# Kernel optimization log

Hardware: AMD Instinct MI355X
Metric: run time of the kernel (lower is better)

## Reference

```python
import jax, jax.numpy as jnp
import numpy as np

B, N, DIM, H, DH = 4, 2048, 768, 12, 64

def layer_norm_no_affine(x, eps=1e-5):
    mu = jnp.mean(x, axis=-1, keepdims=True)
    var = jnp.var(x, axis=-1, keepdims=True)
    return (x - mu) / jnp.sqrt(var + eps)

def setup_inputs() -> dict:
    key = jax.random.key(0)
    ks = jax.random.split(key, 6)
    s = 1.0 / np.sqrt(DIM)
    return {
        "x": jax.random.normal(ks[0], (B, N, DIM), dtype=jnp.float32),
        "gamma": jnp.zeros((DIM,), dtype=jnp.float32),
        "Wq": jax.random.normal(ks[1], (DIM, DIM), dtype=jnp.float32) * s,
        "Wk": jax.random.normal(ks[2], (DIM, DIM), dtype=jnp.float32) * s,
        "Wv": jax.random.normal(ks[3], (DIM, DIM), dtype=jnp.float32) * s,
        "Wo": jax.random.normal(ks[4], (DIM, DIM), dtype=jnp.float32) * s,
    }

def reference(x, gamma, Wq, Wk, Wv, Wo):
    scale = DH ** -0.5
    xn = layer_norm_no_affine(x) * (gamma + 1.0)  # [b,n,dim]
    # projections (torch Linear: y = x @ W.T), split heads b n (h d) -> b h n d
    def proj(t, W):
        return (t @ W.T).reshape(B, N, H, DH).transpose(0, 2, 1, 3)
    q = proj(xn, Wq) * scale
    k = proj(xn, Wk)
    v = proj(xn, Wv)
    qk_sim = jnp.einsum('bhid,bhjd->bhij', q, k)  # full N x N scores (unfused)
    attn = jax.nn.softmax(qk_sim, axis=-1)
    out = jnp.einsum('bhij,bhjd->bhid', attn, v)
    out = out.transpose(0, 2, 1, 3).reshape(B, N, H * DH)
    return out @ Wo.T
```

## Files before the change

kernel.cpp:

```cpp
#include <hip/hip_runtime.h>
#include <stdint.h>

#define NSEQ 2048
#define NB 4
#define NH 12
#define MTOT 8192
#define DMODEL 768

typedef __attribute__((ext_vector_type(8))) short bfx8;
typedef __attribute__((ext_vector_type(4))) float fx4;
typedef __attribute__((ext_vector_type(16))) float fx16;

static __device__ __forceinline__ unsigned short f2bf(float f) {
  union { float f; unsigned u; } v; v.f = f;
  unsigned r = v.u + 0x7FFFu + ((v.u >> 16) & 1u);
  return (unsigned short)(r >> 16);
}

static __device__ __forceinline__ unsigned cvt_pk_bf16(float lo, float hi) {
  unsigned r;
  asm("v_cvt_pk_bf16_f32 %0, %1, %2" : "=v"(r) : "v"(lo), "v"(hi));
  return r;
}

static __device__ __forceinline__ void gload_lds16(const void* g, void* l) {
  __builtin_amdgcn_global_load_lds(
      (const __attribute__((address_space(1))) unsigned int*)g,
      (__attribute__((address_space(3))) unsigned int*)l, 16, 0, 0);
}

__global__ __launch_bounds__(256) void k_ln(const float* __restrict__ x,
                                            const float* __restrict__ gamma,
                                            unsigned short* __restrict__ xn) {
  int row = blockIdx.x * 4 + (threadIdx.x >> 6);
  int lane = threadIdx.x & 63;
  const float* xr = x + (size_t)row * DMODEL;
  float4 a = *(const float4*)(xr + lane * 4);
  float4 b = *(const float4*)(xr + 256 + lane * 4);
  float4 c = *(const float4*)(xr + 512 + lane * 4);
  float s  = a.x + a.y + a.z + a.w + b.x + b.y + b.z + b.w + c.x + c.y + c.z + c.w;
  float ss = a.x*a.x + a.y*a.y + a.z*a.z + a.w*a.w
           + b.x*b.x + b.y*b.y + b.z*b.z + b.w*b.w
           + c.x*c.x + c.y*c.y + c.z*c.z + c.w*c.w;
  #pragma unroll
  for (int off = 1; off < 64; off <<= 1) {
    s  += __shfl_xor(s, off);
    ss += __shfl_xor(ss, off);
  }
  float mu = s * (1.0f / 768.0f);
  float var = ss * (1.0f / 768.0f) - mu * mu;
  float rs = rsqrtf(var + 1e-5f);
  float4 ga = *(const float4*)(gamma + lane * 4);
  float4 gb = *(const float4*)(gamma + 256 + lane * 4);
  float4 gc = *(const float4*)(gamma + 512 + lane * 4);
  unsigned short* orow = xn + (size_t)row * DMODEL;
  ushort4 o;
  o.x = f2bf((a.x - mu) * rs * (ga.x + 1.0f));
  o.y = f2bf((a.y - mu) * rs * (ga.y + 1.0f));
  o.z = f2bf((a.z - mu) * rs * (ga.z + 1.0f));
  o.w = f2bf((a.w - mu) * rs * (ga.w + 1.0f));
  *(ushort4*)(orow + lane * 4) = o;
  o.x = f2bf((b.x - mu) * rs * (gb.x + 1.0f));
  o.y = f2bf((b.y - mu) * rs * (gb.y + 1.0f));
  o.z = f2bf((b.z - mu) * rs * (gb.z + 1.0f));
  o.w = f2bf((b.w - mu) * rs * (gb.w + 1.0f));
  *(ushort4*)(orow + 256 + lane * 4) = o;
  o.x = f2bf((c.x - mu) * rs * (gc.x + 1.0f));
  o.y = f2bf((c.y - mu) * rs * (gc.y + 1.0f));
  o.z = f2bf((c.z - mu) * rs * (gc.z + 1.0f));
  o.w = f2bf((c.w - mu) * rs * (gc.w + 1.0f));
  *(ushort4*)(orow + 512 + lane * 4) = o;
}

__global__ __launch_bounds__(256) void k_wconv(const float* __restrict__ w0,
                                               const float* __restrict__ w1,
                                               const float* __restrict__ w2,
                                               const float* __restrict__ w3,
                                               unsigned short* __restrict__ dst) {
  int which = blockIdx.y;
  const float* src = (which == 0) ? w0 : (which == 1) ? w1 : (which == 2) ? w2 : w3;
  size_t idx = ((size_t)blockIdx.x * 256 + threadIdx.x) * 4;
  float4 v = *(const float4*)(src + idx);
  ushort4 o;
  o.x = f2bf(v.x); o.y = f2bf(v.y); o.z = f2bf(v.z); o.w = f2bf(v.w);
  *(ushort4*)(dst + (size_t)which * (DMODEL * DMODEL) + idx) = o;
}

template<int MODE>
__global__ __launch_bounds__(256) void k_gemm(const unsigned short* __restrict__ A,
                                              const unsigned short* __restrict__ Bbase,
                                              unsigned short* __restrict__ q_o,
                                              unsigned short* __restrict__ k_o,
                                              unsigned short* __restrict__ v_o,
                                              float* __restrict__ f_o) {
  __shared__ unsigned short At[128 * 32];
  __shared__ unsigned short Bt[128 * 32];
  int t = threadIdx.x;
  int w = t >> 6, lane = t & 63;
  int wr = w >> 1, wc = w & 1;
  int g = lane >> 4, cc = lane & 15;
  int mbase = blockIdx.x * 128;
  int by = blockIdx.y;
  const unsigned short* Bp;
  int ncolbase;
  if (MODE == 0) {
    int which = by / 6;
    Bp = Bbase + (size_t)which * (DMODEL * DMODEL);
    ncolbase = (by % 6) * 128;
  } else {
    Bp = Bbase;
    ncolbase = by * 128;
  }
  int srow = lane >> 2;
  int schunk = (lane & 3) * 8;
  const unsigned short* Asrc = A  + (size_t)(mbase   + w * 32 + srow) * DMODEL + schunk;
  const unsigned short* Bsrc = Bp + (size_t)(ncolbase + w * 32 + srow) * DMODEL + schunk;
  unsigned short* Adst0 = At + (w * 32) * 32;
  unsigned short* Bdst0 = Bt + (w * 32) * 32;

  fx4 acc[4][4];
  #pragma unroll
  for (int i = 0; i < 4; ++i)
    #pragma unroll
    for (int j = 0; j < 4; ++j)
      acc[i][j] = (fx4){0.f, 0.f, 0.f, 0.f};

  for (int ks = 0; ks < DMODEL; ks += 32) {
    __syncthreads();
    gload_lds16(Asrc + ks,                    Adst0);
    gload_lds16(Asrc + ks + 16 * DMODEL,      Adst0 + 16 * 32);
    gload_lds16(Bsrc + ks,                    Bdst0);
    gload_lds16(Bsrc + ks + 16 * DMODEL,      Bdst0 + 16 * 32);
    __syncthreads();
    bfx8 af[4], bfr[4];
    #pragma unroll
    for (int mi = 0; mi < 4; ++mi)
      af[mi] = *(const bfx8*)(At + (wr * 64 + mi * 16 + cc) * 32 + g * 8);
    #pragma unroll
    for (int ni = 0; ni < 4; ++ni)
      bfr[ni] = *(const bfx8*)(Bt + (wc * 64 + ni * 16 + cc) * 32 + g * 8);
    #pragma unroll
    for (int mi = 0; mi < 4; ++mi)
      #pragma unroll
      for (int ni = 0; ni < 4; ++ni)
        acc[mi][ni] = __builtin_amdgcn_mfma_f32_16x16x32_bf16(af[mi], bfr[ni], acc[mi][ni], 0, 0, 0);
  }

  if (MODE == 0) {
    int which = by / 6;
    if (which < 2) {
      unsigned short* dst = (which == 0) ? q_o : k_o;
      float fs = (which == 0) ? 0.18033688f : 1.0f;
      #pragma unroll
      for (int mi = 0; mi < 4; ++mi) {
        #pragma unroll
        for (int ni = 0; ni < 4; ++ni) {
          int n = (by % 6) * 128 + wc * 64 + ni * 16 + cc;
          int h = n >> 6, dd = n & 63;
          #pragma unroll
          for (int r = 0; r < 4; ++r) {
            int m = mbase + wr * 64 + mi * 16 + g * 4 + r;
            int bb = m >> 11, nq = m & 2047;
            dst[((size_t)(bb * NH + h) * NSEQ + nq) * 64 + dd] = f2bf(acc[mi][ni][r] * fs);
          }
        }
      }
    } else {
      #pragma unroll
      for (int mi = 0; mi < 4; ++mi) {
        #pragma unroll
        for (int ni = 0; ni < 4; ++ni) {
          int n = (by % 6) * 128 + wc * 64 + ni * 16 + cc;
          int h = n >> 6, dd = n & 63;
          int m0 = mbase + wr * 64 + mi * 16 + g * 4;
          int bb = m0 >> 11, nq = m0 & 2047;
          ushort4 pk;
          pk.x = f2bf(acc[mi][ni][0]);
          pk.y = f2bf(acc[mi][ni][1]);
          pk.z = f2bf(acc[mi][ni][2]);
          pk.w = f2bf(acc[mi][ni][3]);
          *(ushort4*)(v_o + ((size_t)(bb * NH + h) * 64 + dd) * NSEQ + nq) = pk;
        }
      }
    }
  } else {
    #pragma unroll
    for (int mi = 0; mi < 4; ++mi)
      #pragma unroll
      for (int ni = 0; ni < 4; ++ni) {
        int n = by * 128 + wc * 64 + ni * 16 + cc;
        #pragma unroll
        for (int r = 0; r < 4; ++r) {
          int m = mbase + wr * 64 + mi * 16 + g * 4 + r;
          f_o[(size_t)m * DMODEL + n] = acc[mi][ni][r];
        }
      }
  }
}

__global__ __launch_bounds__(256, 3) void k_attn(const unsigned short* __restrict__ qw,
                                                 const unsigned short* __restrict__ kw,
                                                 const unsigned short* __restrict__ vtw,
                                                 unsigned short* __restrict__ ao) {
  __shared__ unsigned short Kb[2][64 * 64];
  __shared__ unsigned short Vb[2][64 * 64];
  int bid = blockIdx.x;
  int xcd = bid & 7, jj = bid >> 3;
  int bh = xcd * 6 + (jj >> 4);
  int qt = jj & 15;
  int t = threadIdx.x;
  int w = t >> 6, lane = t & 63;
  int c = lane & 31, b5 = lane >> 5;
  int q0 = qt * 128 + w * 32;
  const unsigned short* qp = qw + (size_t)bh * NSEQ * 64;
  const unsigned char* kby = (const unsigned char*)(kw  + (size_t)bh * NSEQ * 64);
  const unsigned char* vby = (const unsigned char*)(vtw + (size_t)bh * 64 * NSEQ);

  int srow = lane >> 3;
  int scol = (((lane & 7) ^ srow) << 4);
  int ch0 = 2 * w, ch1 = 2 * w + 1;

  auto stage = [&](int tt, int buf) {
    gload_lds16(kby + (size_t)(tt * 64 + ch0 * 8 + srow) * 128 + scol, &Kb[buf][ch0 * 512]);
    gload_lds16(kby + (size_t)(tt * 64 + ch1 * 8 + srow) * 128 + scol, &Kb[buf][ch1 * 512]);
    gload_lds16(vby + (size_t)(ch0 * 8 + srow) * 4096 + tt * 128 + scol, &Vb[buf][ch0 * 512]);
    gload_lds16(vby + (size_t)(ch1 * 8 + srow) * 4096 + tt * 128 + scol, &Vb[buf][ch1 * 512]);
  };

  bfx8 qf[4];
  #pragma unroll
  for (int dc = 0; dc < 4; ++dc)
    qf[dc] = *(const bfx8*)(qp + (size_t)(q0 + c) * 64 + dc * 16 + b5 * 8);

  fx16 o0, o1;
  #pragma unroll
  for (int i = 0; i < 16; ++i) { o0[i] = 0.f; o1[i] = 0.f; }
  float l_run = 0.f;

  int rsw = (c & 7) << 4;

  stage(0, 0);

  for (int tt = 0; tt < 32; ++tt) {
    int buf = tt & 1;
    __syncthreads();
    if (tt + 1 < 32) stage(tt + 1, buf ^ 1);

    const unsigned char* Kbb = (const unsigned char*)&Kb[buf][0];
    const unsigned char* Vbb = (const unsigned char*)&Vb[buf][0];

    fx16 s0, s1;
    #pragma unroll
    for (int i = 0; i < 16; ++i) { s0[i] = 0.f; s1[i] = 0.f; }
    __builtin_amdgcn_s_setprio(1);
    #pragma unroll
    for (int dc = 0; dc < 4; ++dc) {
      bfx8 kf0 = *(const bfx8*)(Kbb + (c) * 128       + ((dc * 32 + b5 * 16) ^ rsw));
      bfx8 kf1 = *(const bfx8*)(Kbb + (32 + c) * 128  + ((dc * 32 + b5 * 16) ^ rsw));
      s0 = __builtin_amdgcn_mfma_f32_32x32x16_bf16(kf0, qf[dc], s0, 0, 0, 0);
      s1 = __builtin_amdgcn_mfma_f32_32x32x16_bf16(kf1, qf[dc], s1, 0, 0, 0);
    }
    __builtin_amdgcn_s_setprio(0);

    #pragma unroll
    for (int i = 0; i < 16; ++i) {
      s0[i] = __builtin_amdgcn_exp2f(s0[i]);
      s1[i] = __builtin_amdgcn_exp2f(s1[i]);
    }
    float ps = 0.f;
    #pragma unroll
    for (int i = 0; i < 16; ++i) ps += s0[i] + s1[i];
    ps += __shfl_xor(ps, 32);
    l_run += ps;

    bfx8 pf[4];
    #pragma unroll
    for (int half = 0; half < 2; ++half) {
      {
        unsigned w0 = cvt_pk_bf16(s0[8 * half + 0], s0[8 * half + 1]);
        unsigned w1 = cvt_pk_bf16(s0[8 * half + 2], s0[8 * half + 3]);
        unsigned w2 = cvt_pk_bf16(s0[8 * half + 4], s0[8 * half + 5]);
        unsigned w3 = cvt_pk_bf16(s0[8 * half + 6], s0[8 * half + 7]);
        asm("v_permlane32_swap_b32 %0, %1" : "+v"(w0), "+v"(w2));
        asm("v_permlane32_swap_b32 %0, %1" : "+v"(w1), "+v"(w3));
        uint4 u = make_uint4(w0, w1, w2, w3);
        pf[half] = *(bfx8*)&u;
      }
      {
        unsigned w0 = cvt_pk_bf16(s1[8 * half + 0], s1[8 * half + 1]);
        unsigned w1 = cvt_pk_bf16(s1[8 * half + 2], s1[8 * half + 3]);
        unsigned w2 = cvt_pk_bf16(s1[8 * half + 4], s1[8 * half + 5]);
        unsigned w3 = cvt_pk_bf16(s1[8 * half + 6], s1[8 * half + 7]);
        asm("v_permlane32_swap_b32 %0, %1" : "+v"(w0), "+v"(w2));
        asm("v_permlane32_swap_b32 %0, %1" : "+v"(w1), "+v"(w3));
        uint4 u = make_uint4(w0, w1, w2, w3);
        pf[2 + half] = *(bfx8*)&u;
      }
    }

    __builtin_amdgcn_s_setprio(1);
    #pragma unroll
    for (int kc = 0; kc < 4; ++kc) {
      bfx8 vf0 = *(const bfx8*)(Vbb + (c) * 128      + ((kc * 32 + b5 * 16) ^ rsw));
      bfx8 vf1 = *(const bfx8*)(Vbb + (32 + c) * 128 + ((kc * 32 + b5 * 16) ^ rsw));
      o0 = __builtin_amdgcn_mfma_f32_32x32x16_bf16(vf0, pf[kc], o0, 0, 0, 0);
      o1 = __builtin_amdgcn_mfma_f32_32x32x16_bf16(vf1, pf[kc], o1, 0, 0, 0);
    }
    __builtin_amdgcn_s_setprio(0);
  }

  float inv = 1.0f / l_run;
  int b = bh / NH, h = bh % NH;
  unsigned short* orow = ao + (size_t)(b * NSEQ + q0 + c) * DMODEL + h * 64;
  #pragma unroll
  for (int k = 0; k < 4; ++k) {
    ushort4 pk;
    pk.x = f2bf(o0[4 * k + 0] * inv);
    pk.y = f2bf(o0[4 * k + 1] * inv);
    pk.z = f2bf(o0[4 * k + 2] * inv);
    pk.w = f2bf(o0[4 * k + 3] * inv);
    *(ushort4*)(orow + 8 * k + 4 * b5) = pk;
    pk.x = f2bf(o1[4 * k + 0] * inv);
    pk.y = f2bf(o1[4 * k + 1] * inv);
    pk.z = f2bf(o1[4 * k + 2] * inv);
    pk.w = f2bf(o1[4 * k + 3] * inv);
    *(ushort4*)(orow + 32 + 8 * k + 4 * b5) = pk;
  }
}

extern "C" void kernel_launch(void* const* d_in, const int* in_sizes, int n_in,
                              void* d_out, int out_size, void* d_ws, size_t ws_size,
                              hipStream_t stream) {
  const float* x     = (const float*)d_in[0];
  const float* gamma = (const float*)d_in[1];
  const float* Wq    = (const float*)d_in[2];
  const float* Wk    = (const float*)d_in[3];
  const float* Wv    = (const float*)d_in[4];
  const float* Wo    = (const float*)d_in[5];
  float* out = (float*)d_out;

  unsigned short* xn  = (unsigned short*)d_ws;
  unsigned short* wbf = xn  + (size_t)MTOT * DMODEL;
  unsigned short* qws = wbf + (size_t)4 * DMODEL * DMODEL;
  unsigned short* kws = qws + (size_t)MTOT * DMODEL;
  unsigned short* vtws = kws + (size_t)MTOT * DMODEL;
  unsigned short* aow = vtws + (size_t)MTOT * DMODEL;

  k_ln<<<MTOT / 4, 256, 0, stream>>>(x, gamma, xn);
  k_wconv<<<dim3(576, 4), 256, 0, stream>>>(Wq, Wk, Wv, Wo, wbf);
  k_gemm<0><<<dim3(64, 18), 256, 0, stream>>>(xn, wbf, qws, kws, vtws, nullptr);
  k_attn<<<768, 256, 0, stream>>>(qws, kws, vtws, aow);
  k_gemm<1><<<dim3(64, 6), 256, 0, stream>>>(aow, wbf + (size_t)3 * DMODEL * DMODEL,
                                             nullptr, nullptr, nullptr, out);
}
```

Before: 154.7 us.

## Software-pipeline attention QK with previous tile softmax/PV and double-buffer GEMM LDS

Attention is restructured so that the QK^T MFMA for key tile t is issued before the softmax and PV of tile t-1. Two score register sets alternate, and V gets a triple-buffered LDS ring so the prefetch does not overwrite data still in use. The projection GEMM gets double-buffered LDS tiles with a single barrier per k-step, prefetching the next slice while computing the current one. This adds register pressure from the extra score accumulators and more LDS. It also removes the barrier that previously made the GEMM wait for loads to land, which may expose a race.

```diff
diff --git a/kernel.cpp b/kernel.cpp
--- a/kernel.cpp
+++ b/kernel.cpp
@@ -93,8 +93,8 @@
                                               unsigned short* __restrict__ k_o,
                                               unsigned short* __restrict__ v_o,
                                               float* __restrict__ f_o) {
-  __shared__ unsigned short At[128 * 32];
-  __shared__ unsigned short Bt[128 * 32];
+  __shared__ unsigned short At[2][128 * 32];
+  __shared__ unsigned short Bt[2][128 * 32];
   int t = threadIdx.x;
   int w = t >> 6, lane = t & 63;
   int wr = w >> 1, wc = w & 1;
@@ -115,8 +115,13 @@
   int schunk = (lane & 3) * 8;
   const unsigned short* Asrc = A  + (size_t)(mbase   + w * 32 + srow) * DMODEL + schunk;
   const unsigned short* Bsrc = Bp + (size_t)(ncolbase + w * 32 + srow) * DMODEL + schunk;
-  unsigned short* Adst0 = At + (w * 32) * 32;
-  unsigned short* Bdst0 = Bt + (w * 32) * 32;
+
+  auto stage = [&](int ks, int buf) {
+    gload_lds16(Asrc + ks,               &At[buf][(w * 32) * 32]);
+    gload_lds16(Asrc + ks + 16 * DMODEL, &At[buf][(w * 32 + 16) * 32]);
+    gload_lds16(Bsrc + ks,               &Bt[buf][(w * 32) * 32]);
+    gload_lds16(Bsrc + ks + 16 * DMODEL, &Bt[buf][(w * 32 + 16) * 32]);
+  };
 
   fx4 acc[4][4];
   #pragma unroll
@@ -125,20 +130,18 @@
     for (int j = 0; j < 4; ++j)
       acc[i][j] = (fx4){0.f, 0.f, 0.f, 0.f};
 
+  stage(0, 0);
   for (int ks = 0; ks < DMODEL; ks += 32) {
+    int buf = (ks >> 5) & 1;
     __syncthreads();
-    gload_lds16(Asrc + ks,                    Adst0);
-    gload_lds16(Asrc + ks + 16 * DMODEL,      Adst0 + 16 * 32);
-    gload_lds16(Bsrc + ks,                    Bdst0);
-    gload_lds16(Bsrc + ks + 16 * DMODEL,      Bdst0 + 16 * 32);
-    __syncthreads();
+    if (ks + 32 < DMODEL) stage(ks + 32, buf ^ 1);
     bfx8 af[4], bfr[4];
     #pragma unroll
     for (int mi = 0; mi < 4; ++mi)
-      af[mi] = *(const bfx8*)(At + (wr * 64 + mi * 16 + cc) * 32 + g * 8);
+      af[mi] = *(const bfx8*)(&At[buf][(wr * 64 + mi * 16 + cc) * 32 + g * 8]);
     #pragma unroll
     for (int ni = 0; ni < 4; ++ni)
-      bfr[ni] = *(const bfx8*)(Bt + (wc * 64 + ni * 16 + cc) * 32 + g * 8);
+      bfr[ni] = *(const bfx8*)(&Bt[buf][(wc * 64 + ni * 16 + cc) * 32 + g * 8]);
     #pragma unroll
     for (int mi = 0; mi < 4; ++mi)
       #pragma unroll
@@ -203,7 +206,7 @@
                                                  const unsigned short* __restrict__ vtw,
                                                  unsigned short* __restrict__ ao) {
   __shared__ unsigned short Kb[2][64 * 64];
-  __shared__ unsigned short Vb[2][64 * 64];
+  __shared__ unsigned short Vb[3][64 * 64];
   int bid = blockIdx.x;
   int xcd = bid & 7, jj = bid >> 3;
   int bh = xcd * 6 + (jj >> 4);
@@ -220,9 +223,11 @@
   int scol = (((lane & 7) ^ srow) << 4);
   int ch0 = 2 * w, ch1 = 2 * w + 1;
 
-  auto stage = [&](int tt, int buf) {
+  auto stageK = [&](int tt, int buf) {
     gload_lds16(kby + (size_t)(tt * 64 + ch0 * 8 + srow) * 128 + scol, &Kb[buf][ch0 * 512]);
     gload_lds16(kby + (size_t)(tt * 64 + ch1 * 8 + srow) * 128 + scol, &Kb[buf][ch1 * 512]);
+  };
+  auto stageV = [&](int tt, int buf) {
     gload_lds16(vby + (size_t)(ch0 * 8 + srow) * 4096 + tt * 128 + scol, &Vb[buf][ch0 * 512]);
     gload_lds16(vby + (size_t)(ch1 * 8 + srow) * 4096 + tt * 128 + scol, &Vb[buf][ch1 * 512]);
   };
@@ -236,68 +241,61 @@
   #pragma unroll
   for (int i = 0; i < 16; ++i) { o0[i] = 0.f; o1[i] = 0.f; }
   float l_run = 0.f;
-
   int rsw = (c & 7) << 4;
 
-  stage(0, 0);
-
-  for (int tt = 0; tt < 32; ++tt) {
-    int buf = tt & 1;
-    __syncthreads();
-    if (tt + 1 < 32) stage(tt + 1, buf ^ 1);
-
-    const unsigned char* Kbb = (const unsigned char*)&Kb[buf][0];
-    const unsigned char* Vbb = (const unsigned char*)&Vb[buf][0];
-
-    fx16 s0, s1;
-    #pragma unroll
-    for (int i = 0; i < 16; ++i) { s0[i] = 0.f; s1[i] = 0.f; }
+  fx16 sA0, sA1, sB0, sB1;
+
+  auto qk = [&](int tt, fx16& d0, fx16& d1) {
+    const unsigned char* Kbb = (const unsigned char*)&Kb[tt & 1][0];
+    #pragma unroll
+    for (int i = 0; i < 16; ++i) { d0[i] = 0.f; d1[i] = 0.f; }
     __builtin_amdgcn_s_setprio(1);
     #pragma unroll
     for (int dc = 0; dc < 4; ++dc) {
-      bfx8 kf0 = *(const bfx8*)(Kbb + (c) * 128       + ((dc * 32 + b5 * 16) ^ rsw));
-      bfx8 kf1 = *(const bfx8*)(Kbb + (32 + c) * 128  + ((dc * 32 + b5 * 16) ^ rsw));
-      s0 = __builtin_amdgcn_mfma_f32_32x32x16_bf16(kf0, qf[dc], s0, 0, 0, 0);
-      s1 = __builtin_amdgcn_mfma_f32_32x32x16_bf16(kf1, qf[dc], s1, 0, 0, 0);
+      bfx8 kf0 = *(const bfx8*)(Kbb + (c) * 128      + ((dc * 32 + b5 * 16) ^ rsw));
+      bfx8 kf1 = *(const bfx8*)(Kbb + (32 + c) * 128 + ((dc * 32 + b5 * 16) ^ rsw));
+      d0 = __builtin_amdgcn_mfma_f32_32x32x16_bf16(kf0, qf[dc], d0, 0, 0, 0);
+      d1 = __builtin_amdgcn_mfma_f32_32x32x16_bf16(kf1, qf[dc], d1, 0, 0, 0);
     }
     __builtin_amdgcn_s_setprio(0);
-
+  };
+
+  auto softmax_pv = [&](int pv_t, fx16& p0, fx16& p1) {
     #pragma unroll
     for (int i = 0; i < 16; ++i) {
-      s0[i] = __builtin_amdgcn_exp2f(s0[i]);
-      s1[i] = __builtin_amdgcn_exp2f(s1[i]);
+      p0[i] = __builtin_amdgcn_exp2f(p0[i]);
+      p1[i] = __builtin_amdgcn_exp2f(p1[i]);
     }
     float ps = 0.f;
     #pragma unroll
-    for (int i = 0; i < 16; ++i) ps += s0[i] + s1[i];
+    for (int i = 0; i < 16; ++i) ps += p0[i] + p1[i];
     ps += __shfl_xor(ps, 32);
     l_run += ps;
-
     bfx8 pf[4];
     #pragma unroll
     for (int half = 0; half < 2; ++half) {
       {
-        unsigned w0 = cvt_pk_bf16(s0[8 * half + 0], s0[8 * half + 1]);
-        unsigned w1 = cvt_pk_bf16(s0[8 * half + 2], s0[8 * half + 3]);
-        unsigned w2 = cvt_pk_bf16(s0[8 * half + 4], s0[8 * half + 5]);
-        unsigned w3 = cvt_pk_bf16(s0[8 * half + 6], s0[8 * half + 7]);
+        unsigned w0 = cvt_pk_bf16(p0[8 * half + 0], p0[8 * half + 1]);
+        unsigned w1 = cvt_pk_bf16(p0[8 * half + 2], p0[8 * half + 3]);
+        unsigned w2 = cvt_pk_bf16(p0[8 * half + 4], p0[8 * half + 5]);
+        unsigned w3 = cvt_pk_bf16(p0[8 * half + 6], p0[8 * half + 7]);
         asm("v_permlane32_swap_b32 %0, %1" : "+v"(w0), "+v"(w2));
         asm("v_permlane32_swap_b32 %0, %1" : "+v"(w1), "+v"(w3));
         uint4 u = make_uint4(w0, w1, w2, w3);
         pf[half] = *(bfx8*)&u;
       }
       {
-        unsigned w0 = cvt_pk_bf16(s1[8 * half + 0], s1[8 * half + 1]);
-        unsigned w1 = cvt_pk_bf16(s1[8 * half + 2], s1[8 * half + 3]);
-        unsigned w2 = cvt_pk_bf16(s1[8 * half + 4], s1[8 * half + 5]);
-        unsigned w3 = cvt_pk_bf16(s1[8 * half + 6], s1[8 * half + 7]);
+        unsigned w0 = cvt_pk_bf16(p1[8 * half + 0], p1[8 * half + 1]);
+        unsigned w1 = cvt_pk_bf16(p1[8 * half + 2], p1[8 * half + 3]);
+        unsigned w2 = cvt_pk_bf16(p1[8 * half + 4], p1[8 * half + 5]);
+        unsigned w3 = cvt_pk_bf16(p1[8 * half + 6], p1[8 * half + 7]);
         asm("v_permlane32_swap_b32 %0, %1" : "+v"(w0), "+v"(w2));
         asm("v_permlane32_swap_b32 %0, %1" : "+v"(w1), "+v"(w3));
         uint4 u = make_uint4(w0, w1, w2, w3);
         pf[2 + half] = *(bfx8*)&u;
       }
     }
-
+    const unsigned char* Vbb = (const unsigned char*)&Vb[pv_t % 3][0];
     __builtin_amdgcn_s_setprio(1);
     #pragma unroll
     for (int kc = 0; kc < 4; ++kc) {
@@ -307,7 +305,26 @@
       o1 = __builtin_amdgcn_mfma_f32_32x32x16_bf16(vf1, pf[kc], o1, 0, 0, 0);
     }
     __builtin_amdgcn_s_setprio(0);
-  }
+  };
+
+  auto body = [&](int tt, fx16& cur0, fx16& cur1, fx16& prv0, fx16& prv1) {
+    __syncthreads();
+    qk(tt, cur0, cur1);
+    if (tt + 1 < 32) { stageK(tt + 1, (tt + 1) & 1); stageV(tt + 1, (tt + 1) % 3); }
+    softmax_pv(tt - 1, prv0, prv1);
+  };
+
+  stageK(0, 0); stageV(0, 0);
+  __syncthreads();
+  qk(0, sA0, sA1);
+  stageK(1, 1); stageV(1, 1);
+
+  for (int tp = 1; tp < 31; tp += 2) {
+    body(tp,     sB0, sB1, sA0, sA1);
+    body(tp + 1, sA0, sA1, sB0, sB1);
+  }
+  body(31, sB0, sB1, sA0, sA1);
+  softmax_pv(31, sB0, sB1);
 
   float inv = 1.0f / l_run;
   int b = bh / NH, h = bh % NH;
```

After: 141.5 us. 1.09x faster.
